# Optimization experiments

Hardware: AMD Instinct MI355X
Metric: run time of the kernel (lower is better)

## Reference

```python
import jax, jax.numpy as jnp
import numpy as np

FEATURES = 8
POINTS = 3
CLASSES = 128
BATCH = 1024
TEMPERATURE = 0.1


def setup_inputs() -> dict:
    key = jax.random.key(0)
    k1, k2, k3 = jax.random.split(key, 3)
    x = jax.random.normal(k1, (BATCH, FEATURES), dtype=jnp.float32)
    beta = jax.random.uniform(k2, (FEATURES, POINTS), dtype=jnp.float32)
    classifier = jax.random.uniform(
        k3, ((POINTS + 1) ** FEATURES, CLASSES), dtype=jnp.float32)
    return {"x": x, "beta": beta, "classifier": classifier}


def reference(x, beta, classifier):
    # b: sort beta ascending per-feature, negate, cumsum, prepend a zero bin edge
    T = 1.0 / TEMPERATURE
    bneg = jnp.cumsum(-jnp.sort(beta, axis=1), axis=1)            # [F, P]
    b = jnp.concatenate(
        [jnp.zeros((beta.shape[0], 1), beta.dtype), bneg], axis=1)  # [F, P+1]
    w = jnp.arange(1, POINTS + 2, dtype=x.dtype)                  # [P+1]
    # soft one-hot binning per feature: [B, F, P+1]
    logits = (x[:, :, None] * w[None, None, :] + b[None, :, :]) * T
    hot = jax.nn.softmax(logits, axis=-1)
    # iterative outer product over features -> joint leaf histogram [B, (P+1)^F]
    B = x.shape[0]
    leaves = hot[:, 0, :]
    for f in range(1, FEATURES):  # small fixed loop over features
        leaves = (leaves[:, :, None] * hot[:, f, None, :]).reshape(B, -1)
    return leaves @ classifier  # [B, classes]
```

## Files before the change

### kernel.cpp

```cpp
#include <hip/hip_runtime.h>
#include <stdint.h>

typedef unsigned short u16;
typedef __attribute__((ext_vector_type(4))) float f32x4;
typedef __attribute__((ext_vector_type(2))) float f32x2;
typedef __attribute__((ext_vector_type(8))) short s16x8;

#define T_INV 10.0f

__device__ __forceinline__ u16 f2bf(float f) {
  uint32_t u = __float_as_uint(f);
  uint32_t r = (u + 0x7FFFu + ((u >> 16) & 1u)) >> 16;
  return (u16)r;
}

__device__ __forceinline__ void gload_lds16(const void* g, void* l) {
  __builtin_amdgcn_global_load_lds(
      (const __attribute__((address_space(1))) uint32_t*)(g),
      (__attribute__((address_space(3))) uint32_t*)(l),
      16, 0, 0);
}

__global__ __launch_bounds__(256) void k_prep(
    const float* __restrict__ cls, const float* __restrict__ x,
    const float* __restrict__ beta,
    u16* __restrict__ ct, u16* __restrict__ plo, float* __restrict__ phiT)
{
  const int t = threadIdx.x;
  if (blockIdx.x < 1024) {
    __shared__ float tile[64 * 132];
    const int k0 = blockIdx.x * 64;
#pragma unroll
    for (int it = 0; it < 8; ++it) {
      int e = it * 1024 + t * 4;
      int r = e >> 7;
      int c = e & 127;
      f32x4 v = *(const f32x4*)(cls + (size_t)(k0 + r) * 128 + c);
      *(f32x4*)(tile + r * 132 + c) = v;
    }
    __syncthreads();
    const int c  = t >> 1;
    const int kh = t & 1;
    u16 vals[32];
#pragma unroll
    for (int j = 0; j < 32; ++j)
      vals[j] = f2bf(tile[(kh*32 + j) * 132 + c]);
    u16* dst = ct + ((size_t)(k0 >> 3) + kh * 4) * 1024 + c * 8;
#pragma unroll
    for (int qq = 0; qq < 4; ++qq) {
      s16x8 v;
#pragma unroll
      for (int e2 = 0; e2 < 8; ++e2) v[e2] = (short)vals[qq*8 + e2];
      *(s16x8*)(dst + (size_t)qq * 1024) = v;
    }
  } else {
    const int b = (blockIdx.x - 1024) * 64 + (t >> 2);
    const int q = t & 3;
    float hot[8][4];
#pragma unroll
    for (int f = 0; f < 8; ++f) {
      float b0 = beta[f*3+0], b1 = beta[f*3+1], b2 = beta[f*3+2];
      float s0 = fminf(b0, fminf(b1, b2));
      float s2 = fmaxf(b0, fmaxf(b1, b2));
      float s1 = b0 + b1 + b2 - s0 - s2;
      float bv1 = -s0, bv2 = -(s0 + s1), bv3 = -(s0 + s1 + s2);
      float xf = x[b*8 + f];
      float l0 = (xf * 1.0f       ) * T_INV;
      float l1 = (xf * 2.0f + bv1) * T_INV;
      float l2 = (xf * 3.0f + bv2) * T_INV;
      float l3 = (xf * 4.0f + bv3) * T_INV;
      float mm = fmaxf(fmaxf(l0, l1), fmaxf(l2, l3));
      float e0 = __expf(l0 - mm), e1 = __expf(l1 - mm);
      float e2 = __expf(l2 - mm), e3 = __expf(l3 - mm);
      float inv = 1.0f / (e0 + e1 + e2 + e3);
      hot[f][0] = e0*inv; hot[f][1] = e1*inv; hot[f][2] = e2*inv; hot[f][3] = e3*inv;
    }
    {
      float h23[16];
#pragma unroll
      for (int i2 = 0; i2 < 4; ++i2)
#pragma unroll
        for (int i3 = 0; i3 < 4; ++i3) h23[i2*4+i3] = hot[2][i2] * hot[3][i3];
      float h0q = hot[0][q];
#pragma unroll
      for (int i1 = 0; i1 < 4; ++i1) {
        float c01 = h0q * hot[1][i1];
#pragma unroll
        for (int j = 0; j < 16; ++j)
          phiT[(size_t)(q*64 + i1*16 + j) * 1024 + b] = c01 * h23[j];
      }
    }
    {
      float h67[16];
#pragma unroll
      for (int i6 = 0; i6 < 4; ++i6)
#pragma unroll
        for (int i7 = 0; i7 < 4; ++i7) h67[i6*4+i7] = hot[6][i6] * hot[7][i7];
      float h4q = hot[4][q];
      u16* dst = plo + (size_t)b*256 + q*64;
#pragma unroll
      for (int i5 = 0; i5 < 4; ++i5) {
        float c45 = h4q * hot[5][i5];
#pragma unroll
        for (int j = 0; j < 16; j += 8) {
          s16x8 v;
#pragma unroll
          for (int e = 0; e < 8; ++e) v[e] = (short)f2bf(c45 * h67[j+e]);
          *(s16x8*)(dst + i5*16 + j) = v;
        }
      }
    }
  }
}

__global__ __launch_bounds__(256, 2) void k_main(
    const u16* __restrict__ plo, const float* __restrict__ phiT,
    const u16* __restrict__ ct, u16* __restrict__ pws)
{
  __shared__ __align__(16) u16 As[32768];

  const int wg  = blockIdx.x;
  const int xcd = wg & 7;
  const int idx = wg >> 3;
  const int hig = xcd * 8 + (idx >> 3);
  const int m   = idx & 7;

  const int t    = threadIdx.x;
  const int l    = t & 63;
  const int w    = t >> 6;
  const int lrow = l & 15;
  const int kg   = l >> 4;
  const int rbase = (w & 1) * 64;
  const int cbase = (w >> 1) * 64;

  const u16* ploM = plo + (size_t)m * 128 * 256;

#pragma unroll
  for (int i = 0; i < 16; ++i) {
    int ks  = i >> 1;
    int row = (i & 1) * 64 + (t >> 2);
    int g   = ((t & 3) - ((t >> 3) & 3)) & 3;
    gload_lds16(ploM + (size_t)row * 256 + ks * 32 + g * 8, &As[i * 2048 + t * 8]);
  }
  __builtin_amdgcn_sched_barrier(0);
  asm volatile("s_waitcnt vmcnt(0)" ::: "memory");
  __builtin_amdgcn_sched_barrier(0);
  __builtin_amdgcn_s_barrier();
  __builtin_amdgcn_sched_barrier(0);

  const u16* bW = ct + (size_t)hig * 131072 + (size_t)kg * 1024
                     + (size_t)(cbase + lrow) * 8;

  f32x4 acc[4][4], hacc[4][4];
#pragma unroll
  for (int i = 0; i < 4; ++i)
#pragma unroll
    for (int j = 0; j < 4; ++j) { acc[i][j] = (f32x4)0.0f; hacc[i][j] = (f32x4)0.0f; }

  s16x8 bE[4], bO[4];
#pragma unroll
  for (int nt = 0; nt < 4; ++nt) bE[nt] = *(const s16x8*)(bW + nt * 128);

#pragma unroll 1
  for (int h = 0; h < 4; ++h) {
    const u16* bh = bW + (size_t)h * 32768;
#pragma unroll
    for (int ks2 = 0; ks2 < 4; ++ks2) {
      const int ksA = ks2 * 2, ksB = ksA + 1;
#pragma unroll
      for (int nt = 0; nt < 4; ++nt)
        bO[nt] = *(const s16x8*)(bh + ksB * 4096 + nt * 128);
      {
        s16x8 afr[4];
        const u16* Ak = &As[ksA * 4096];
#pragma unroll
        for (int mt = 0; mt < 4; ++mt) {
          int row = rbase + mt * 16 + lrow;
          int s = (kg + ((row >> 1) & 3)) & 3;
          afr[mt] = *(const s16x8*)(Ak + row * 32 + s * 8);
        }
#pragma unroll
        for (int mt = 0; mt < 4; ++mt)
#pragma unroll
          for (int nt = 0; nt < 4; ++nt)
            hacc[mt][nt] = __builtin_amdgcn_mfma_f32_16x16x32_bf16(
                afr[mt], bE[nt], hacc[mt][nt], 0, 0, 0);
      }
      if (ks2 < 3) {
#pragma unroll
        for (int nt = 0; nt < 4; ++nt)
          bE[nt] = *(const s16x8*)(bh + (ksA + 2) * 4096 + nt * 128);
      } else if (h < 3) {
#pragma unroll
        for (int nt = 0; nt < 4; ++nt)
          bE[nt] = *(const s16x8*)(bh + 32768 + nt * 128);
      }
      {
        s16x8 afr[4];
        const u16* Ak = &As[ksB * 4096];
#pragma unroll
        for (int mt = 0; mt < 4; ++mt) {
          int row = rbase + mt * 16 + lrow;
          int s = (kg + ((row >> 1) & 3)) & 3;
          afr[mt] = *(const s16x8*)(Ak + row * 32 + s * 8);
        }
#pragma unroll
        for (int mt = 0; mt < 4; ++mt)
#pragma unroll
          for (int nt = 0; nt < 4; ++nt)
            hacc[mt][nt] = __builtin_amdgcn_mfma_f32_16x16x32_bf16(
                afr[mt], bO[nt], hacc[mt][nt], 0, 0, 0);
      }
    }
#pragma unroll
    for (int mt = 0; mt < 4; ++mt) {
      f32x4 p4 = *(const f32x4*)(phiT + (size_t)(hig * 4 + h) * 1024
                                 + m * 128 + rbase + mt * 16 + kg * 4);
#pragma unroll
      for (int r = 0; r < 4; ++r)
#pragma unroll
        for (int nt = 0; nt < 4; ++nt)
          acc[mt][nt][r] += p4[r] * hacc[mt][nt][r];
#pragma unroll
      for (int nt = 0; nt < 4; ++nt) hacc[mt][nt] = (f32x4)0.0f;
    }
  }

  __syncthreads();
  {
    u16* ob = As;
#pragma unroll
    for (int mt = 0; mt < 4; ++mt)
#pragma unroll
      for (int r = 0; r < 4; ++r) {
        int row = rbase + mt * 16 + kg * 4 + r;
#pragma unroll
        for (int nt = 0; nt < 4; ++nt) {
          int col = cbase + nt * 16 + lrow;
          ob[row * 136 + col] = f2bf(acc[mt][nt][r]);
        }
      }
    __syncthreads();
    const int row  = t >> 1;
    const int half = t & 1;
    const u16* srcp = ob + row * 136 + half * 64;
    u16* gdst = pws + ((size_t)hig * 1024 + (size_t)m * 128) * 128
                    + row * 128 + half * 64;
#pragma unroll
    for (int i = 0; i < 8; ++i)
      *(s16x8*)(gdst + i * 8) = *(const s16x8*)(srcp + i * 8);
  }
}

__global__ __launch_bounds__(256) void k_reduce(
    const u16* __restrict__ p, float* __restrict__ out)
{
  const int g = blockIdx.x * 256 + threadIdx.x;
  const u16* src = p + (size_t)g * 2;
  float a0 = 0.0f, a1 = 0.0f;
#pragma unroll 8
  for (int hig = 0; hig < 64; ++hig) {
    uint32_t v = *(const uint32_t*)(src + (size_t)hig * 131072);
    a0 += __uint_as_float((v & 0xFFFFu) << 16);
    a1 += __uint_as_float(v & 0xFFFF0000u);
  }
  f32x2 o; o.x = a0; o.y = a1;
  *(f32x2*)(out + (size_t)g * 2) = o;
}

extern "C" void kernel_launch(void* const* d_in, const int* in_sizes, int n_in,
                              void* d_out, int out_size, void* d_ws, size_t ws_size,
                              hipStream_t stream)
{
  const float* x    = (const float*)d_in[0];
  const float* beta = (const float*)d_in[1];
  const float* cls  = (const float*)d_in[2];
  float* out = (float*)d_out;

  char* ws = (char*)d_ws;
  u16*   ct   = (u16*)ws;
  u16*   plo  = (u16*)(ws + (16u << 20));
  float* phiT = (float*)(ws + (16u << 20) + 524288);
  u16*   pws  = (u16*)(ws + (16u << 20) + 524288 + 1048576);

  k_prep<<<1040, 256, 0, stream>>>(cls, x, beta, ct, plo, phiT);
  k_main<<<512, 256, 0, stream>>>(plo, phiT, ct, pws);
  k_reduce<<<256, 256, 0, stream>>>(pws, out);
}
```

Baseline: 56.55 us.

## Fold per-h phi scaling into a running ratio to drop separate hacc accumulators

Rather than keeping a second set of accumulators (hacc) per h block and adding phi*hacc into acc, the kernel accumulates directly into acc and rescales it by the ratio phi_prev/phi_next between h blocks, with a final multiply by the last phi. This frees 64 accumulator registers per thread and removes the zeroing and add pass. The cost is extra rcp and multiplies, plus an epsilon clamp on phi that can change numerics when phi is tiny. It also switches the launch-bounds hint to amdgpu_waves_per_eu(2, 2) and uses nontemporal stores and loads for the partial-sum buffer.

```diff
diff --git a/kernel.cpp b/kernel.cpp
--- a/kernel.cpp
+++ b/kernel.cpp
@@ -7,6 +7,7 @@
 typedef __attribute__((ext_vector_type(8))) short s16x8;
 
 #define T_INV 10.0f
+#define QEPS 9.5367431640625e-07f
 
 __device__ __forceinline__ u16 f2bf(float f) {
   uint32_t u = __float_as_uint(f);
@@ -113,7 +114,9 @@
   }
 }
 
-__global__ __launch_bounds__(256, 2) void k_main(
+__global__ __launch_bounds__(256)
+__attribute__((amdgpu_waves_per_eu(2, 2)))
+void k_main(
     const u16* __restrict__ plo, const float* __restrict__ phiT,
     const u16* __restrict__ ct, u16* __restrict__ pws)
 {
@@ -151,11 +154,22 @@
   const u16* bW = ct + (size_t)hig * 131072 + (size_t)kg * 1024
                      + (size_t)(cbase + lrow) * 8;
 
-  f32x4 acc[4][4], hacc[4][4];
+  f32x4 qprev[4];
+  {
+    const float* p0 = phiT + (size_t)(hig * 4) * 1024 + m * 128;
+#pragma unroll
+    for (int mt = 0; mt < 4; ++mt) {
+      f32x4 q = *(const f32x4*)(p0 + rbase + mt * 16 + kg * 4);
+#pragma unroll
+      for (int r = 0; r < 4; ++r) qprev[mt][r] = fmaxf(q[r], QEPS);
+    }
+  }
+
+  f32x4 acc[4][4];
 #pragma unroll
   for (int i = 0; i < 4; ++i)
 #pragma unroll
-    for (int j = 0; j < 4; ++j) { acc[i][j] = (f32x4)0.0f; hacc[i][j] = (f32x4)0.0f; }
+    for (int j = 0; j < 4; ++j) acc[i][j] = (f32x4)0.0f;
 
   s16x8 bE[4], bO[4];
 #pragma unroll
@@ -183,8 +197,8 @@
         for (int mt = 0; mt < 4; ++mt)
 #pragma unroll
           for (int nt = 0; nt < 4; ++nt)
-            hacc[mt][nt] = __builtin_amdgcn_mfma_f32_16x16x32_bf16(
-                afr[mt], bE[nt], hacc[mt][nt], 0, 0, 0);
+            acc[mt][nt] = __builtin_amdgcn_mfma_f32_16x16x32_bf16(
+                afr[mt], bE[nt], acc[mt][nt], 0, 0, 0);
       }
       if (ks2 < 3) {
 #pragma unroll
@@ -208,21 +222,28 @@
         for (int mt = 0; mt < 4; ++mt)
 #pragma unroll
           for (int nt = 0; nt < 4; ++nt)
-            hacc[mt][nt] = __builtin_amdgcn_mfma_f32_16x16x32_bf16(
-                afr[mt], bO[nt], hacc[mt][nt], 0, 0, 0);
-      }
-    }
-#pragma unroll
-    for (int mt = 0; mt < 4; ++mt) {
-      f32x4 p4 = *(const f32x4*)(phiT + (size_t)(hig * 4 + h) * 1024
-                                 + m * 128 + rbase + mt * 16 + kg * 4);
-#pragma unroll
-      for (int r = 0; r < 4; ++r)
+            acc[mt][nt] = __builtin_amdgcn_mfma_f32_16x16x32_bf16(
+                afr[mt], bO[nt], acc[mt][nt], 0, 0, 0);
+      }
+    }
+    if (h < 3) {
+      const float* pn = phiT + (size_t)(hig * 4 + h + 1) * 1024 + m * 128;
+#pragma unroll
+      for (int mt = 0; mt < 4; ++mt) {
+        f32x4 qn = *(const f32x4*)(pn + rbase + mt * 16 + kg * 4);
+        f32x4 ratio;
+#pragma unroll
+        for (int r = 0; r < 4; ++r) {
+          float q = fmaxf(qn[r], QEPS);
+          ratio[r] = qprev[mt][r] * __builtin_amdgcn_rcpf(q);
+          qprev[mt][r] = q;
+        }
 #pragma unroll
         for (int nt = 0; nt < 4; ++nt)
-          acc[mt][nt][r] += p4[r] * hacc[mt][nt][r];
-#pragma unroll
-      for (int nt = 0; nt < 4; ++nt) hacc[mt][nt] = (f32x4)0.0f;
+#pragma unroll
+          for (int r = 0; r < 4; ++r)
+            acc[mt][nt][r] *= ratio[r];
+      }
     }
   }
 
@@ -237,7 +258,7 @@
 #pragma unroll
         for (int nt = 0; nt < 4; ++nt) {
           int col = cbase + nt * 16 + lrow;
-          ob[row * 136 + col] = f2bf(acc[mt][nt][r]);
+          ob[row * 136 + col] = f2bf(acc[mt][nt][r] * qprev[mt][r]);
         }
       }
     __syncthreads();
@@ -248,7 +269,8 @@
                     + row * 128 + half * 64;
 #pragma unroll
     for (int i = 0; i < 8; ++i)
-      *(s16x8*)(gdst + i * 8) = *(const s16x8*)(srcp + i * 8);
+      __builtin_nontemporal_store(*(const s16x8*)(srcp + i * 8),
+                                  (s16x8*)(gdst + i * 8));
   }
 }
 
@@ -260,7 +282,8 @@
   float a0 = 0.0f, a1 = 0.0f;
 #pragma unroll 8
   for (int hig = 0; hig < 64; ++hig) {
-    uint32_t v = *(const uint32_t*)(src + (size_t)hig * 131072);
+    uint32_t v = __builtin_nontemporal_load(
+        (const uint32_t*)(src + (size_t)hig * 131072));
     a0 += __uint_as_float((v & 0xFFFFu) << 16);
     a1 += __uint_as_float(v & 0xFFFF0000u);
   }
```

Result: slower. 75.18 us (+33.0%).
